# Performance work log

Measured on AMD Instinct MI355X. Metric: run time of the kernel, lower is better.

## Reference

```python
import jax, jax.numpy as jnp
import numpy as np

P = 9            # patch_size
HP = P // 2      # half_patch
EMB = 128        # embedding_dim


def setup_inputs() -> dict:
    key = jax.random.key(0)
    ks = jax.random.split(key, 5)
    B, T, H, W, N = 16, 16, 384, 384, 2048
    images = jax.random.normal(ks[0], (B, T, 3, H, W), dtype=jnp.float32)
    coords = jax.random.uniform(ks[1], (B, N, 2), dtype=jnp.float32)
    t_src = jax.random.randint(ks[2], (B, N), 0, T).astype(jnp.int32)
    # conv params (torch Conv2d default has bias)
    W1 = jax.random.normal(ks[3], (64, 3, 3, 3), dtype=jnp.float32) * 0.1
    b1 = jnp.zeros((64,), jnp.float32)
    W2 = jax.random.normal(ks[4], (EMB, 64, P, P), dtype=jnp.float32) * 0.02
    b2 = jnp.zeros((EMB,), jnp.float32)
    return dict(images=images, coords=coords, t_src=t_src, W1=W1, b1=b1, W2=W2, b2=b2)


def _extract_patches(images, coords, t_src):
    """Vectorized version of the per-(b,n) python-loop patch gather."""
    B, T, C, H, W = images.shape
    px = jnp.round(coords * jnp.array([W, H], coords.dtype)).astype(jnp.int32)
    u = jnp.clip(px[..., 0], HP, W - HP - 1)          # (B, N)
    v = jnp.clip(px[..., 1], HP, H - HP - 1)          # (B, N)
    t = jnp.clip(t_src, 0, T - 1).astype(jnp.int32)   # (B, N)

    def slice_one(img_b, t_n, u_n, v_n):
        frame = jax.lax.dynamic_index_in_dim(img_b, t_n, axis=0, keepdims=False)  # (C,H,W)
        return jax.lax.dynamic_slice(frame, (0, v_n - HP, u_n - HP), (img_b.shape[1], P, P))

    per_b = jax.vmap(slice_one, in_axes=(None, 0, 0, 0))   # over N
    patches = jax.vmap(per_b)(images, t, u, v)              # (B, N, C, P, P)
    return patches


def reference(images, coords, t_src, W1, b1, W2, b2):
    B, T, C, H, W = images.shape
    N = coords.shape[1]
    patches = _extract_patches(images, coords, t_src).reshape(B * N, C, P, P)
    dn = ('NCHW', 'OIHW', 'NCHW')
    # Conv2d(3,64,k=3,pad=1) + ReLU
    h = jax.lax.conv_general_dilated(patches, W1, (1, 1), ((1, 1), (1, 1)),
                                     dimension_numbers=dn) + b1[None, :, None, None]
    h = jax.nn.relu(h)
    # Conv2d(64,EMB,k=P,pad=0) -> spatial 1x1; AdaptiveAvgPool2d(1) is identity here
    h = jax.lax.conv_general_dilated(h, W2, (1, 1), 'VALID',
                                     dimension_numbers=dn) + b2[None, :, None, None]
    h = h.mean(axis=(2, 3))  # (B*N, EMB)
    return h.reshape(B, N, EMB)
```

## Files before the change

### kernel.cpp

```cpp
#include <hip/hip_runtime.h>
#include <stdint.h>

#define NTHR 256
#define PP   28
#define HST  104
#define WST  104
#define NPATCH 32768
#define W2B_ELEMS (64*128*WST)
#define HW (384*384)

typedef __attribute__((ext_vector_type(8))) short bf16x8;
typedef __attribute__((ext_vector_type(4))) float f32x4;
typedef uint32_t u32;
typedef uint16_t u16;

__device__ __forceinline__ u16 f2bf(float f){
    u32 x = __float_as_uint(f);
    return (u16)((x + 0x7fffu + ((x >> 16) & 1u)) >> 16);
}
__device__ __forceinline__ u32 pack2(float a, float b){
    return (u32)f2bf(a) | ((u32)f2bf(b) << 16);
}
__device__ __forceinline__ bf16x8 u4bf(uint4 x){
    union { uint4 u; bf16x8 b; } c; c.u = x; return c.b;
}

__global__ void w2_prep(const float* __restrict__ W2, u16* __restrict__ W2b){
    int i = blockIdx.x * 256 + threadIdx.x;
    if (i >= W2B_ELEMS) return;
    int g   = i / (128 * WST);
    int rem = i - g * (128 * WST);
    int oc  = rem / WST;
    int k   = rem - oc * WST;
    u16 v = 0;
    if (k < 81) v = f2bf(W2[(size_t)oc * 5184 + g * 81 + k]);
    W2b[i] = v;
}

template<bool USEWS>
__device__ __forceinline__ void load_B(const u16* __restrict__ W2b,
                                       const float* __restrict__ W2,
                                       int g, int oc0, int oc1, int g4,
                                       uint4 PB[3][2])
{
    if constexpr (USEWS) {
        const u16* base = W2b + (size_t)g * (128 * WST);
        #pragma unroll
        for (int s = 0; s < 3; ++s) {
            const int ko = s * 32 + g4 * 8;
            PB[s][0] = *(const uint4*)(base + oc0 * WST + ko);
            PB[s][1] = *(const uint4*)(base + oc1 * WST + ko);
        }
    } else {
        #pragma unroll
        for (int s = 0; s < 3; ++s) {
            const int ko = s * 32 + g4 * 8;
            #pragma unroll
            for (int half = 0; half < 2; ++half) {
                const float* so = W2 + (size_t)(half ? oc1 : oc0) * 5184 + g * 81;
                u32 q0 = pack2(ko     < 81 ? so[ko]     : 0.f, ko + 1 < 81 ? so[ko + 1] : 0.f);
                u32 q1 = pack2(ko + 2 < 81 ? so[ko + 2] : 0.f, ko + 3 < 81 ? so[ko + 3] : 0.f);
                u32 q2 = pack2(ko + 4 < 81 ? so[ko + 4] : 0.f, ko + 5 < 81 ? so[ko + 5] : 0.f);
                u32 q3 = pack2(ko + 6 < 81 ? so[ko + 6] : 0.f, ko + 7 < 81 ? so[ko + 7] : 0.f);
                PB[s][half] = (uint4){q0, q1, q2, q3};
            }
        }
    }
}

template<bool USEWS>
__global__ __launch_bounds__(NTHR)
void patch_embed(const float* __restrict__ images,
                 const float* __restrict__ coords,
                 const int*   __restrict__ t_src,
                 const float* __restrict__ W1,
                 const float* __restrict__ b1,
                 const float* __restrict__ W2,
                 const u16*   __restrict__ W2b,
                 const float* __restrict__ b2,
                 float* __restrict__ out)
{
    __shared__ __align__(16) u16 Hl[2][32 * HST];
    __shared__ int poff[PP];

    const int tid  = threadIdx.x;
    const int blk  = blockIdx.x;
    const int lane = tid & 63;
    const int w    = tid >> 6;
    const int n16  = lane & 15;
    const int g4   = lane >> 4;

    if (tid < PP) {
        int gp = blk * PP + tid;
        if (gp >= NPATCH) gp = NPATCH - 1;
        int b = gp >> 11;
        int n = gp & 2047;
        float cx = coords[(size_t)(b * 2048 + n) * 2 + 0];
        float cy = coords[(size_t)(b * 2048 + n) * 2 + 1];
        int u = (int)rintf(cx * 384.0f);
        int v = (int)rintf(cy * 384.0f);
        u = min(max(u, 4), 379);
        v = min(max(v, 4), 379);
        int t = t_src[b * 2048 + n];
        t = min(max(t, 0), 15);
        poff[tid] = ((b * 16 + t) * 3) * HW + (v - 4) * 384 + (u - 4);
    }
    {
        u32* Hz = (u32*)Hl;
        #pragma unroll
        for (int j = 0; j < 13; ++j) Hz[tid + j * NTHR] = 0u;
    }
    __syncthreads();

    const bool has = tid < PP * 9;
    const int p0 = has ? tid / 9 : 0;
    const int y0 = has ? tid - 9 * (tid / 9) : 0;
    float rf[3][27];
    {
        const int base = poff[p0];
        #pragma unroll
        for (int dy = 0; dy < 3; ++dy) {
            const int yy = y0 - 1 + dy;
            const bool vrow = has && (yy >= 0) && (yy <= 8);
            #pragma unroll
            for (int j = 0; j < 27; ++j) rf[dy][j] = 0.f;
            if (vrow) {
                #pragma unroll
                for (int c = 0; c < 3; ++c) {
                    const float* rp = images + (size_t)base + c * HW + yy * 384;
                    #pragma unroll
                    for (int x = 0; x < 9; ++x) rf[dy][c * 9 + x] = rp[x];
                }
            }
        }
    }

    const int oc0 = w * 32 + n16;
    const int oc1 = oc0 + 16;
    uint4 PB[3][2];
    load_B<USEWS>(W2b, W2, 0, oc0, oc1, g4, PB);

    f32x4 acc[2][2];
    #pragma unroll
    for (int mt = 0; mt < 2; ++mt)
        #pragma unroll
        for (int nt = 0; nt < 2; ++nt) acc[mt][nt] = (f32x4){0.f, 0.f, 0.f, 0.f};

    #pragma unroll 1
    for (int g = 0; g < 64; ++g) {
        const float* W1c = W1 + (size_t)g * 27;
        const float bias = b1[g];
        u16 h9[9];
        {
            float a[9];
            #pragma unroll
            for (int x = 0; x < 9; ++x) a[x] = bias;
            #pragma unroll
            for (int dy = 0; dy < 3; ++dy) {
                #pragma unroll
                for (int c = 0; c < 3; ++c) {
                    const float* rr = rf[dy] + c * 9;
                    const int wi = c * 9 + dy * 3;
                    const float w0 = W1c[wi], w1 = W1c[wi + 1], w2 = W1c[wi + 2];
                    #pragma unroll
                    for (int xo = 0; xo < 9; ++xo) {
                        a[xo] = fmaf(rr[xo], w1, a[xo]);
                        if (xo >= 1) a[xo] = fmaf(rr[xo - 1], w0, a[xo]);
                        if (xo <= 7) a[xo] = fmaf(rr[xo + 1], w2, a[xo]);
                    }
                }
            }
            #pragma unroll
            for (int xo = 0; xo < 9; ++xo) {
                float v = a[xo] > 0.f ? a[xo] : 0.f;
                h9[xo] = f2bf(v);
            }
        }

        {
            u16* Hb = &Hl[g & 1][0];
            if (has) {
                #pragma unroll
                for (int xo = 0; xo < 9; ++xo) Hb[p0 * HST + y0 * 9 + xo] = h9[xo];
            }
        }

        __syncthreads();

        {
            const u16* Hb = &Hl[g & 1][0];
            #pragma unroll
            for (int s = 0; s < 3; ++s) {
                const int ko = s * 32 + g4 * 8;
                bf16x8 a0  = *(const bf16x8*)(Hb + (n16     ) * HST + ko);
                bf16x8 a1  = *(const bf16x8*)(Hb + (16 + n16) * HST + ko);
                bf16x8 vb0 = u4bf(PB[s][0]);
                bf16x8 vb1 = u4bf(PB[s][1]);
                acc[0][0] = __builtin_amdgcn_mfma_f32_16x16x32_bf16(a0, vb0, acc[0][0], 0, 0, 0);
                acc[0][1] = __builtin_amdgcn_mfma_f32_16x16x32_bf16(a0, vb1, acc[0][1], 0, 0, 0);
                acc[1][0] = __builtin_amdgcn_mfma_f32_16x16x32_bf16(a1, vb0, acc[1][0], 0, 0, 0);
                acc[1][1] = __builtin_amdgcn_mfma_f32_16x16x32_bf16(a1, vb1, acc[1][1], 0, 0, 0);
            }
        }

        if (g < 63) load_B<USEWS>(W2b, W2, g + 1, oc0, oc1, g4, PB);
    }

    const float bias0 = b2[oc0];
    const float bias1 = b2[oc1];
    #pragma unroll
    for (int mt = 0; mt < 2; ++mt) {
        #pragma unroll
        for (int r = 0; r < 4; ++r) {
            int p = mt * 16 + g4 * 4 + r;
            int gp = blk * PP + p;
            if (p < PP && gp < NPATCH) {
                size_t rowo = (size_t)gp * 128;
                out[rowo + oc0] = acc[mt][0][r] + bias0;
                out[rowo + oc1] = acc[mt][1][r] + bias1;
            }
        }
    }
}

extern "C" void kernel_launch(void* const* d_in, const int* in_sizes, int n_in,
                              void* d_out, int out_size, void* d_ws, size_t ws_size,
                              hipStream_t stream)
{
    const float* images = (const float*)d_in[0];
    const float* coords = (const float*)d_in[1];
    const int*   t_src  = (const int*)d_in[2];
    const float* W1     = (const float*)d_in[3];
    const float* b1     = (const float*)d_in[4];
    const float* W2     = (const float*)d_in[5];
    const float* b2     = (const float*)d_in[6];
    float* out = (float*)d_out;
    u16* W2b = (u16*)d_ws;

    const int grid = (NPATCH + PP - 1) / PP;
    const bool usews = ws_size >= (size_t)W2B_ELEMS * sizeof(u16);

    if (usews) {
        hipLaunchKernelGGL(w2_prep, dim3((W2B_ELEMS + 255) / 256), dim3(256), 0, stream,
                           W2, W2b);
        hipLaunchKernelGGL(patch_embed<true>, dim3(grid), dim3(NTHR), 0, stream,
                           images, coords, t_src, W1, b1, W2, W2b, b2, out);
    } else {
        hipLaunchKernelGGL(patch_embed<false>, dim3(grid), dim3(NTHR), 0, stream,
                           images, coords, t_src, W1, b1, W2, W2b, b2, out);
    }
}
```

Baseline: 241.3 us.

## Split conv1 channels across two blocks per patch group with atomic accumulation

Each patch group is now processed by two blocks, each covering half of the 64 intermediate channels (split-K over the second conv's reduction). The partial sums are combined with float atomicAdd into an output that is zeroed by a memset, and only the first half adds the bias. This doubles the grid and halves the per-block serial loop to improve latency hiding and occupancy. In exchange, both blocks reload the image patches, and the change adds a memset, atomic traffic and non-deterministic summation order.

```diff
diff --git a/kernel.cpp b/kernel.cpp
--- a/kernel.cpp
+++ b/kernel.cpp
@@ -6,6 +6,7 @@
 #define HST  104
 #define WST  104
 #define NPATCH 32768
+#define CHALF 32
 #define W2B_ELEMS (64*128*WST)
 #define HW (384*384)
 
@@ -41,7 +42,7 @@
 __device__ __forceinline__ void load_B(const u16* __restrict__ W2b,
                                        const float* __restrict__ W2,
                                        int g, int oc0, int oc1, int g4,
-                                       uint4 PB[3][2])
+                                       uint4 (&PB)[3][2])
 {
     if constexpr (USEWS) {
         const u16* base = W2b + (size_t)g * (128 * WST);
@@ -84,14 +85,16 @@
     __shared__ int poff[PP];
 
     const int tid  = threadIdx.x;
-    const int blk  = blockIdx.x;
+    const int pb   = blockIdx.x >> 1;
+    const int half = blockIdx.x & 1;
+    const int hbase = half * CHALF;
     const int lane = tid & 63;
     const int w    = tid >> 6;
     const int n16  = lane & 15;
     const int g4   = lane >> 4;
 
     if (tid < PP) {
-        int gp = blk * PP + tid;
+        int gp = pb * PP + tid;
         if (gp >= NPATCH) gp = NPATCH - 1;
         int b = gp >> 11;
         int n = gp & 2047;
@@ -138,7 +141,7 @@
     const int oc0 = w * 32 + n16;
     const int oc1 = oc0 + 16;
     uint4 PB[3][2];
-    load_B<USEWS>(W2b, W2, 0, oc0, oc1, g4, PB);
+    load_B<USEWS>(W2b, W2, hbase, oc0, oc1, g4, PB);
 
     f32x4 acc[2][2];
     #pragma unroll
@@ -147,9 +150,10 @@
         for (int nt = 0; nt < 2; ++nt) acc[mt][nt] = (f32x4){0.f, 0.f, 0.f, 0.f};
 
     #pragma unroll 1
-    for (int g = 0; g < 64; ++g) {
-        const float* W1c = W1 + (size_t)g * 27;
-        const float bias = b1[g];
+    for (int g = 0; g < CHALF; ++g) {
+        const int c = hbase + g;
+        const float* W1c = W1 + (size_t)c * 27;
+        const float bias = b1[c];
         u16 h9[9];
         {
             float a[9];
@@ -158,9 +162,9 @@
             #pragma unroll
             for (int dy = 0; dy < 3; ++dy) {
                 #pragma unroll
-                for (int c = 0; c < 3; ++c) {
-                    const float* rr = rf[dy] + c * 9;
-                    const int wi = c * 9 + dy * 3;
+                for (int cc = 0; cc < 3; ++cc) {
+                    const float* rr = rf[dy] + cc * 9;
+                    const int wi = cc * 9 + dy * 3;
                     const float w0 = W1c[wi], w1 = W1c[wi + 1], w2 = W1c[wi + 2];
                     #pragma unroll
                     for (int xo = 0; xo < 9; ++xo) {
@@ -203,21 +207,21 @@
             }
         }
 
-        if (g < 63) load_B<USEWS>(W2b, W2, g + 1, oc0, oc1, g4, PB);
-    }
-
-    const float bias0 = b2[oc0];
-    const float bias1 = b2[oc1];
+        if (g < CHALF - 1) load_B<USEWS>(W2b, W2, c + 1, oc0, oc1, g4, PB);
+    }
+
+    const float bias0 = half == 0 ? b2[oc0] : 0.f;
+    const float bias1 = half == 0 ? b2[oc1] : 0.f;
     #pragma unroll
     for (int mt = 0; mt < 2; ++mt) {
         #pragma unroll
         for (int r = 0; r < 4; ++r) {
             int p = mt * 16 + g4 * 4 + r;
-            int gp = blk * PP + p;
+            int gp = pb * PP + p;
             if (p < PP && gp < NPATCH) {
                 size_t rowo = (size_t)gp * 128;
-                out[rowo + oc0] = acc[mt][0][r] + bias0;
-                out[rowo + oc1] = acc[mt][1][r] + bias1;
+                atomicAdd(out + rowo + oc0, acc[mt][0][r] + bias0);
+                atomicAdd(out + rowo + oc1, acc[mt][1][r] + bias1);
             }
         }
     }
@@ -237,7 +241,9 @@
     float* out = (float*)d_out;
     u16* W2b = (u16*)d_ws;
 
-    const int grid = (NPATCH + PP - 1) / PP;
+    hipMemsetAsync(out, 0, (size_t)out_size * sizeof(float), stream);
+
+    const int grid = 2 * ((NPATCH + PP - 1) / PP);
     const bool usews = ws_size >= (size_t)W2B_ELEMS * sizeof(u16);
 
     if (usews) {
```

After: 270.8 us. 12.2% more time.
